# Optimization experiments

Measured on AMD Instinct MI355X. Metric: run time of the kernel, lower is better.

Reference implementation:

```python
import jax, jax.numpy as jnp
import numpy as np
import math

NUM_HEADS = 32
NUM_KV = 8
D = 128          # num_hidden == per-head dim in this module
S = 2048
B = 1
DK = 128
ROPE_BASE = 10000.0


def rope(x):
    # x: [B, H, S, D]; standard Llama-style RoPE (split-halves rotation) over positions.
    d = x.shape[-1]
    half = d // 2
    pos = jnp.arange(x.shape[2], dtype=jnp.float32)                       # [S]
    inv_freq = 1.0 / (ROPE_BASE ** (jnp.arange(half, dtype=jnp.float32) / half))
    ang = pos[:, None] * inv_freq[None, :]                                # [S, half]
    cos = jnp.cos(ang)
    sin = jnp.sin(ang)
    x1 = x[..., :half]
    x2 = x[..., half:]
    return jnp.concatenate([x1 * cos - x2 * sin, x1 * sin + x2 * cos], axis=-1)


def setup_inputs() -> dict:
    key = jax.random.key(0)
    ks = jax.random.split(key, 8)
    query = jax.random.normal(ks[0], (B, S, D), dtype=jnp.float32)
    k_in = jax.random.normal(ks[1], (B, S, D), dtype=jnp.float32)
    v_in = jax.random.normal(ks[2], (B, S, D), dtype=jnp.float32)
    # causal mask: 1 where attention allowed (lower triangle incl diagonal)
    mask = jnp.tril(jnp.ones((S, S), dtype=jnp.int32))[None, None]        # [1,1,S,S]
    sc = 0.02
    Wq = jax.random.normal(ks[3], (NUM_HEADS * D, D), dtype=jnp.float32) * sc
    bq = jnp.zeros((NUM_HEADS * D,), dtype=jnp.float32)
    Wk = jax.random.normal(ks[4], (NUM_KV * D, D), dtype=jnp.float32) * sc
    bk = jnp.zeros((NUM_KV * D,), dtype=jnp.float32)
    Wv = jax.random.normal(ks[5], (NUM_KV * D, D), dtype=jnp.float32) * sc
    bv = jnp.zeros((NUM_KV * D,), dtype=jnp.float32)
    Wo = jax.random.normal(ks[6], (D, NUM_HEADS * D), dtype=jnp.float32) * sc
    bo = jnp.zeros((D,), dtype=jnp.float32)
    return {"query": query, "key": k_in, "values": v_in, "mask": mask,
            "Wq": Wq, "bq": bq, "Wk": Wk, "bk": bk, "Wv": Wv, "bv": bv,
            "Wo": Wo, "bo": bo}


def reference(query, key, values, mask, Wq, bq, Wk, bk, Wv, bv, Wo, bo):
    Bq, Sq, Dh = query.shape
    # projections; torch Linear: x @ W.T + b. Note: view (reshape), not transpose,
    # exactly as in the original module.
    q = (query @ Wq.T + bq).reshape(Bq, NUM_HEADS, Sq, Dh)   # [B,H,S,D]
    k = (key @ Wk.T + bk).reshape(Bq, NUM_KV, Sq, Dh)        # [B,Hkv,S,D]
    v = (values @ Wv.T + bv).reshape(Bq, NUM_KV, Sq, Dh)
    rk = rope(k)
    rv = rope(v)  # module applies RoPE to values too (faithful)
    rep = NUM_HEADS // NUM_KV
    # torch .repeat((1, rep, 1, 1)) tiles whole head blocks -> jnp.tile
    rk = jnp.tile(rk, (1, rep, 1, 1))                        # [B,H,S,D]
    rv = jnp.tile(rv, (1, rep, 1, 1))
    scores = jnp.einsum('bhqd,bhkd->bhqk', q, rk) / math.sqrt(DK)
    scores = jnp.where(mask == 0, -jnp.inf, scores)
    attn = jax.nn.softmax(scores, axis=-1)
    out = jnp.einsum('bhqk,bhkd->bhqd', attn, rv)            # [B,H,S,D]
    out = out.transpose(0, 2, 1, 3).reshape(Bq, Sq, NUM_HEADS * Dh)
    return out @ Wo.T + bo
```

## Files before the change

### kernel.cpp

```cpp
#include <hip/hip_runtime.h>

typedef unsigned short u16;
typedef unsigned int u32;
typedef short frag_t __attribute__((ext_vector_type(8)));
typedef float f32x4 __attribute__((ext_vector_type(4)));

#define S_LEN 2048

__device__ __forceinline__ float bf2f(u32 u) {
  union { u32 i; float f; } v; v.i = u << 16; return v.f;
}
__device__ __forceinline__ u16 f2bf(float f) {
  u32 x = __float_as_uint(f);
  u32 r = (x + 0x7fffu + ((x >> 16) & 1u)) >> 16;
  return (u16)r;
}
__device__ __forceinline__ void unpack8(uint4 r, float* o) {
  o[0] = bf2f(r.x & 0xffffu); o[1] = bf2f(r.x >> 16);
  o[2] = bf2f(r.y & 0xffffu); o[3] = bf2f(r.y >> 16);
  o[4] = bf2f(r.z & 0xffffu); o[5] = bf2f(r.z >> 16);
  o[6] = bf2f(r.w & 0xffffu); o[7] = bf2f(r.w >> 16);
}
__device__ __forceinline__ u16 ld_in(const void* p, size_t idx, bool fp32) {
  if (fp32) return f2bf(((const float*)p)[idx]);
  return ((const u16*)p)[idx];
}
__device__ __forceinline__ uint4 ld8(const void* p, size_t eidx, bool fp32) {
  if (!fp32) return *(const uint4*)((const u16*)p + eidx);
  const float4* f = (const float4*)((const float*)p + eidx);
  float4 x = f[0], y = f[1];
  uint4 r;
  r.x = (u32)f2bf(x.x) | ((u32)f2bf(x.y) << 16);
  r.y = (u32)f2bf(x.z) | ((u32)f2bf(x.w) << 16);
  r.z = (u32)f2bf(y.x) | ((u32)f2bf(y.y) << 16);
  r.w = (u32)f2bf(y.z) | ((u32)f2bf(y.w) << 16);
  return r;
}

__global__ void detect_dtype(const u16* __restrict__ q, u32* __restrict__ flag) {
  int t = threadIdx.x;
  u32 e = ((u32)q[2 * t] >> 7) & 0xFFu;
  bool ok = (e >= 110u && e <= 140u);
  unsigned long long b = __ballot(ok);
  if (t == 0) *flag = (__popcll(b) < 32) ? 1u : 0u;
}

__global__ __launch_bounds__(256) void proj_all(
    const void* __restrict__ query, const void* __restrict__ key,
    const void* __restrict__ values,
    const void* __restrict__ Wq, const void* __restrict__ bq,
    const void* __restrict__ Wk, const void* __restrict__ bk,
    const void* __restrict__ Wv, const void* __restrict__ bv,
    u16* __restrict__ Qb, u16* __restrict__ Kb, u16* __restrict__ Vtmp,
    const u32* __restrict__ flagp) {
  __shared__ u16 As[64][136];
  __shared__ u16 Ws[64][136];
  u16 (*Cs)[72] = (u16(*)[72])&As[0][0];
  const bool fp32 = (*flagp != 0u);
  const int t = threadIdx.x;
  const int x = blockIdx.x;
  const void *A, *W, *bias;
  u16* C; int N, n0;
  if (x < 64)      { A = query;  W = Wq; bias = bq; C = Qb;   N = 4096; n0 = x << 6; }
  else if (x < 80) { A = key;    W = Wk; bias = bk; C = Kb;   N = 1024; n0 = (x - 64) << 6; }
  else             { A = values; W = Wv; bias = bv; C = Vtmp; N = 1024; n0 = (x - 80) << 6; }
  const int m0 = blockIdx.y << 6;
  for (int i = t; i < 1024; i += 256) {
    int r = i >> 4, d8 = (i & 15) << 3;
    *(uint4*)&As[r][d8] = ld8(A, (size_t)(m0 + r) * 128 + d8, fp32);
    *(uint4*)&Ws[r][d8] = ld8(W, (size_t)(n0 + r) * 128 + d8, fp32);
  }
  __syncthreads();
  const int lane = t & 63, w = t >> 6, quad = lane >> 4, l15 = lane & 15;
  f32x4 acc[4];
#pragma unroll
  for (int nt = 0; nt < 4; ++nt) acc[nt] = 0.f;
#pragma unroll
  for (int kc = 0; kc < 4; ++kc) {
    frag_t a = *(const frag_t*)&As[w * 16 + l15][kc * 32 + quad * 8];
#pragma unroll
    for (int nt = 0; nt < 4; ++nt) {
      frag_t b = *(const frag_t*)&Ws[nt * 16 + l15][kc * 32 + quad * 8];
      acc[nt] = __builtin_amdgcn_mfma_f32_16x16x32_bf16(a, b, acc[nt], 0, 0, 0);
    }
  }
  __syncthreads();
#pragma unroll
  for (int nt = 0; nt < 4; ++nt) {
    float bb = bf2f((u32)ld_in(bias, n0 + nt * 16 + l15, fp32));
#pragma unroll
    for (int r = 0; r < 4; ++r)
      Cs[w * 16 + quad * 4 + r][nt * 16 + l15] = f2bf(acc[nt][r] + bb);
  }
  __syncthreads();
#pragma unroll
  for (int jj = 0; jj < 2; ++jj) {
    int c = t + (jj << 8);
    int row = c >> 3, ch = (c & 7) << 3;
    *(uint4*)&C[(size_t)(m0 + row) * N + n0 + ch] = *(const uint4*)&Cs[row][ch];
  }
}

__global__ __launch_bounds__(256) void rope_kv_tr(u16* __restrict__ Kb,
                                                  const u16* __restrict__ Vb,
                                                  u16* __restrict__ VbT) {
  __shared__ u16 Lt[128][72];
  const int t = threadIdx.x;
  const int s0 = blockIdx.x << 6;
  const int g = blockIdx.y;
  for (int i = t; i < 4096; i += 256) {
    int s = s0 + (i >> 6), ii = i & 63;
    float invf = __expf(-(float)ii * 0.14391156831212787f);
    float ang = (float)s * invf;
    float sn, cs;
    sincosf(ang, &sn, &cs);
    size_t base = ((size_t)(g << 11) + s) * 128 + ii;
    float k1 = bf2f((u32)Kb[base]), k2 = bf2f((u32)Kb[base + 64]);
    Kb[base] = f2bf(k1 * cs - k2 * sn);
    Kb[base + 64] = f2bf(k1 * sn + k2 * cs);
  }
  const u16* src = Vb + (size_t)g * S_LEN * 128;
  for (int i = t; i < 512; i += 256) {
    int r = i >> 3, d8 = (i & 7) << 3;
    float lo[8], hi[8];
    unpack8(*(const uint4*)&src[(size_t)(s0 + r) * 128 + d8], lo);
    unpack8(*(const uint4*)&src[(size_t)(s0 + r) * 128 + d8 + 64], hi);
#pragma unroll
    for (int j = 0; j < 8; ++j) {
      float invf = __expf(-(float)(d8 + j) * 0.14391156831212787f);
      float ang = (float)(s0 + r) * invf;
      float sn, cs;
      sincosf(ang, &sn, &cs);
      Lt[d8 + j][r] = f2bf(lo[j] * cs - hi[j] * sn);
      Lt[d8 + 64 + j][r] = f2bf(lo[j] * sn + hi[j] * cs);
    }
  }
  __syncthreads();
  u16* dst = VbT + (size_t)g * 128 * S_LEN + s0;
  for (int i = t; i < 2048; i += 256) {
    int d = i >> 4, s4 = (i & 15) << 2;
    uint2 pk;
    pk.x = (u32)Lt[d][s4] | ((u32)Lt[d][s4 + 1] << 16);
    pk.y = (u32)Lt[d][s4 + 2] | ((u32)Lt[d][s4 + 3] << 16);
    *(uint2*)&dst[(size_t)d * S_LEN + s4] = pk;
  }
}

__global__ __launch_bounds__(512, 2) void attn_mfma(
    const u16* __restrict__ Qb, const u16* __restrict__ Kb,
    const u16* __restrict__ VbT, u16* __restrict__ Ob) {
  __shared__ __align__(16) char smem[102400];
  u16 (*Kt)[64][136] = (u16(*)[64][136])smem;
  u16 (*Vt)[128][72] = (u16(*)[128][72])(smem + 34816);
  u16 (*St)[40]      = (u16(*)[40])(smem + 71680);
  float* Om = (float*)smem;
  float* Ml = (float*)(smem + 65536);
  u16 (*Og)[136]     = (u16(*)[136])(smem + 67584);
  const int t = threadIdx.x;
  const int lane = t & 63, w = t >> 6, quad = lane >> 4, l15 = lane & 15;
  const int hw = w & 3, half = w >> 2;
  const int g = blockIdx.y;
  const int pi = blockIdx.x;
  const int h = g + (hw << 3);
  const u16* Kg = Kb + (size_t)g * S_LEN * 128;
  const u16* Vg = VbT + (size_t)g * 128 * S_LEN;
  const int kr0 = t >> 4, kc0 = (t & 15) << 3;
  const int vr0 = t >> 3, vc0 = (t & 7) << 3;

  for (int tp = 0; tp < 2; ++tp) {
    const int qt = tp ? pi : 63 - pi;
    const int q0 = qt << 5;
    const int niter = qt + 1;
    const int nsuper = (niter + 1) >> 1;
    frag_t aq[2][4];
#pragma unroll
    for (int qp = 0; qp < 2; ++qp)
#pragma unroll
      for (int kc = 0; kc < 4; ++kc)
        aq[qp][kc] = *(const frag_t*)&Qb[((size_t)h * S_LEN + q0 + qp * 16 + l15) * 128 +
                                         kc * 32 + quad * 8];
    float m_r[2] = {-1e30f, -1e30f}, l_r[2] = {0.f, 0.f};
    f32x4 oacc[2][8];
#pragma unroll
    for (int qp = 0; qp < 2; ++qp)
#pragma unroll
      for (int nt = 0; nt < 8; ++nt) oacc[qp][nt] = 0.f;

    uint4 kpf[2], vpf[2];
#pragma unroll
    for (int j = 0; j < 2; ++j) {
      kpf[j] = *(const uint4*)&Kg[(size_t)(kr0 + j * 32) * 128 + kc0];
      vpf[j] = *(const uint4*)&Vg[(size_t)(vr0 + j * 64) * S_LEN + vc0];
    }
#pragma unroll
    for (int j = 0; j < 2; ++j) {
      *(uint4*)&Kt[0][kr0 + j * 32][kc0] = kpf[j];
      *(uint4*)&Vt[0][vr0 + j * 64][vc0] = vpf[j];
    }
    if (nsuper > 1) {
#pragma unroll
      for (int j = 0; j < 2; ++j) {
        kpf[j] = *(const uint4*)&Kg[(size_t)(64 + kr0 + j * 32) * 128 + kc0];
        vpf[j] = *(const uint4*)&Vg[(size_t)(vr0 + j * 64) * S_LEN + 64 + vc0];
      }
    }

    for (int sj = 0; sj < nsuper; ++sj) {
      __syncthreads();
      const int buf = sj & 1;
      if (sj + 1 < nsuper) {
#pragma unroll
        for (int j = 0; j < 2; ++j) {
          *(uint4*)&Kt[buf ^ 1][kr0 + j * 32][kc0] = kpf[j];
          *(uint4*)&Vt[buf ^ 1][vr0 + j * 64][vc0] = vpf[j];
        }
      }
      if (sj + 2 < nsuper) {
        const int kn = (sj + 2) << 6;
#pragma unroll
        for (int j = 0; j < 2; ++j) {
          kpf[j] = *(const uint4*)&Kg[(size_t)(kn + kr0 + j * 32) * 128 + kc0];
          vpf[j] = *(const uint4*)&Vg[(size_t)(vr0 + j * 64) * S_LEN + kn + vc0];
        }
      }
      const int tile32 = (sj << 1) + half;
      if (tile32 < niter) {
        const int kbase = tile32 << 5;
        const int lk = half << 5;
        f32x4 s4[2][2];
#pragma unroll
        for (int kk = 0; kk < 2; ++kk)
#pragma unroll
          for (int qp = 0; qp < 2; ++qp) s4[kk][qp] = 0.f;
#pragma unroll
        for (int kc = 0; kc < 4; ++kc) {
#pragma unroll
          for (int kk = 0; kk < 2; ++kk) {
            frag_t a = *(const frag_t*)&Kt[buf][lk + kk * 16 + l15][kc * 32 + quad * 8];
            s4[kk][0] = __builtin_amdgcn_mfma_f32_16x16x32_bf16(a, aq[0][kc], s4[kk][0], 0, 0, 0);
            s4[kk][1] = __builtin_amdgcn_mfma_f32_16x16x32_bf16(a, aq[1][kc], s4[kk][1], 0, 0, 0);
          }
        }
        const bool lastm = (tile32 == niter - 1);
        float alpha[2];
#pragma unroll
        for (int qp = 0; qp < 2; ++qp) {
          const int qg = q0 + qp * 16 + l15;
          float mx = -1e30f;
#pragma unroll
          for (int kk = 0; kk < 2; ++kk)
#pragma unroll
            for (int r = 0; r < 4; ++r) {
              float sv = s4[kk][qp][r] * 0.08838834764831845f;
              if (lastm && (kbase + kk * 16 + quad * 4 + r) > qg) sv = -1e30f;
              s4[kk][qp][r] = sv;
              mx = fmaxf(mx, sv);
            }
          mx = fmaxf(mx, __shfl_xor(mx, 16));
          mx = fmaxf(mx, __shfl_xor(mx, 32));
          float mn = fmaxf(m_r[qp], mx);
          alpha[qp] = __expf(m_r[qp] - mn);
          m_r[qp] = mn;
          float sum = 0.f;
          const int strow = w * 32 + qp * 16 + l15;
#pragma unroll
          for (int kk = 0; kk < 2; ++kk) {
            float p0 = __expf(s4[kk][qp][0] - mn);
            float p1 = __expf(s4[kk][qp][1] - mn);
            float p2 = __expf(s4[kk][qp][2] - mn);
            float p3 = __expf(s4[kk][qp][3] - mn);
            sum += (p0 + p1) + (p2 + p3);
            uint2 pk;
            pk.x = (u32)f2bf(p0) | ((u32)f2bf(p1) << 16);
            pk.y = (u32)f2bf(p2) | ((u32)f2bf(p3) << 16);
            *(uint2*)&St[strow][kk * 16 + quad * 4] = pk;
          }
          sum += __shfl_xor(sum, 16);
          sum += __shfl_xor(sum, 32);
          l_r[qp] = l_r[qp] * alpha[qp] + sum;
        }
#pragma unroll
        for (int qp = 0; qp < 2; ++qp)
#pragma unroll
          for (int r = 0; r < 4; ++r) {
            float al = __shfl(alpha[qp], quad * 4 + r);
#pragma unroll
            for (int nt = 0; nt < 8; ++nt) oacc[qp][nt][r] *= al;
          }
        frag_t pa[2];
#pragma unroll
        for (int qp = 0; qp < 2; ++qp)
          pa[qp] = *(const frag_t*)&St[w * 32 + qp * 16 + l15][quad * 8];
#pragma unroll
        for (int nt = 0; nt < 8; ++nt) {
          frag_t v = *(const frag_t*)&Vt[buf][nt * 16 + l15][lk + quad * 8];
          oacc[0][nt] = __builtin_amdgcn_mfma_f32_16x16x32_bf16(pa[0], v, oacc[0][nt], 0, 0, 0);
          oacc[1][nt] = __builtin_amdgcn_mfma_f32_16x16x32_bf16(pa[1], v, oacc[1][nt], 0, 0, 0);
        }
      }
    }
    __syncthreads();
    if (half == 1) {
#pragma unroll
      for (int qp = 0; qp < 2; ++qp)
#pragma unroll
        for (int nt = 0; nt < 8; ++nt)
#pragma unroll
          for (int r = 0; r < 4; ++r)
            Om[((hw * 32) + qp * 16 + quad * 4 + r) * 128 + nt * 16 + l15] = oacc[qp][nt][r];
      if (quad == 0) {
#pragma unroll
        for (int qp = 0; qp < 2; ++qp) {
          Ml[hw * 64 + qp * 16 + l15] = m_r[qp];
          Ml[hw * 64 + 32 + qp * 16 + l15] = l_r[qp];
        }
      }
    }
    __syncthreads();
    if (half == 0) {
      float v1[2], v2[2];
#pragma unroll
      for (int qp = 0; qp < 2; ++qp) {
        float m2 = Ml[hw * 64 + qp * 16 + l15];
        float l2 = Ml[hw * 64 + 32 + qp * 16 + l15];
        float mn = fmaxf(m_r[qp], m2);
        float a1 = __expf(m_r[qp] - mn);
        float a2 = __expf(m2 - mn);
        float linv = 1.0f / (a1 * l_r[qp] + a2 * l2);
        v1[qp] = a1 * linv;
        v2[qp] = a2 * linv;
      }
#pragma unroll
      for (int qp = 0; qp < 2; ++qp)
#pragma unroll
        for (int r = 0; r < 4; ++r) {
          float w1 = __shfl(v1[qp], quad * 4 + r);
          float w2 = __shfl(v2[qp], quad * 4 + r);
#pragma unroll
          for (int nt = 0; nt < 8; ++nt) {
            float o2 = Om[((hw * 32) + qp * 16 + quad * 4 + r) * 128 + nt * 16 + l15];
            Og[hw * 32 + qp * 16 + quad * 4 + r][nt * 16 + l15] =
                f2bf(oacc[qp][nt][r] * w1 + o2 * w2);
          }
        }
    }
    __syncthreads();
#pragma unroll
    for (int jj = 0; jj < 4; ++jj) {
      int c = t + (jj << 9);
      int row = c >> 4, ch = (c & 15) << 3;
      int hh = row >> 5, qr = row & 31;
      *(uint4*)&Ob[(size_t)(q0 + qr) * 4096 + (g + hh * 8) * 128 + ch] =
          *(const uint4*)&Og[row][ch];
    }
  }
}

__global__ __launch_bounds__(256) void out_part(
    const u16* __restrict__ Ob, const void* __restrict__ Wo,
    float* __restrict__ Pout, const u32* __restrict__ flagp) {
  __shared__ u16 As[32][72];
  __shared__ u16 Ws[64][72];
  const bool fp32 = (*flagp != 0u);
  const int t = threadIdx.x;
  const int lane = t & 63, w = t >> 6, quad = lane >> 4, l15 = lane & 15;
  const int wm = w & 1, wn = w >> 1;
  const int n0 = (int)blockIdx.x << 6;
  const int m0 = (int)blockIdx.y << 5;
  const int kz = (int)blockIdx.z << 10;
  f32x4 acc[2];
#pragma unroll
  for (int nt = 0; nt < 2; ++nt) acc[nt] = 0.f;
  for (int kc0 = kz; kc0 < kz + 1024; kc0 += 64) {
    if (kc0 != kz) __syncthreads();
    {
      int r = t >> 3, k8 = (t & 7) << 3;
      *(uint4*)&As[r][k8] = *(const uint4*)&Ob[(size_t)(m0 + r) * 4096 + kc0 + k8];
    }
    for (int i = t; i < 512; i += 256) {
      int r = i >> 3, k8 = (i & 7) << 3;
      *(uint4*)&Ws[r][k8] = ld8(Wo, (size_t)(n0 + r) * 4096 + kc0 + k8, fp32);
    }
    __syncthreads();
#pragma unroll
    for (int kc2 = 0; kc2 < 2; ++kc2) {
      frag_t a = *(const frag_t*)&As[wm * 16 + l15][kc2 * 32 + quad * 8];
#pragma unroll
      for (int nt = 0; nt < 2; ++nt) {
        frag_t b = *(const frag_t*)&Ws[wn * 32 + nt * 16 + l15][kc2 * 32 + quad * 8];
        acc[nt] = __builtin_amdgcn_mfma_f32_16x16x32_bf16(a, b, acc[nt], 0, 0, 0);
      }
    }
  }
#pragma unroll
  for (int nt = 0; nt < 2; ++nt) {
    int n = n0 + wn * 32 + nt * 16 + l15;
#pragma unroll
    for (int r = 0; r < 4; ++r) {
      int m = m0 + wm * 16 + quad * 4 + r;
      Pout[((size_t)blockIdx.z * 2048 + m) * 128 + n] = acc[nt][r];
    }
  }
}

__global__ __launch_bounds__(256) void out_red(
    const float* __restrict__ Pout, const void* __restrict__ bo,
    void* __restrict__ out, const u32* __restrict__ flagp) {
  const bool fp32 = (*flagp != 0u);
  int e4 = blockIdx.x * 256 + threadIdx.x;
  const float4* P = (const float4*)Pout;
  float4 s = P[e4];
  float4 s1 = P[65536 + e4], s2 = P[131072 + e4], s3 = P[196608 + e4];
  s.x += s1.x + s2.x + s3.x; s.y += s1.y + s2.y + s3.y;
  s.z += s1.z + s2.z + s3.z; s.w += s1.w + s2.w + s3.w;
  int n = (e4 << 2) & 127;
  s.x += bf2f((u32)ld_in(bo, n + 0, fp32));
  s.y += bf2f((u32)ld_in(bo, n + 1, fp32));
  s.z += bf2f((u32)ld_in(bo, n + 2, fp32));
  s.w += bf2f((u32)ld_in(bo, n + 3, fp32));
  if (fp32) {
    ((float4*)out)[e4] = s;
  } else {
    uint2 pk;
    pk.x = (u32)f2bf(s.x) | ((u32)f2bf(s.y) << 16);
    pk.y = (u32)f2bf(s.z) | ((u32)f2bf(s.w) << 16);
    *(uint2*)((u16*)out + (e4 << 2)) = pk;
  }
}

extern "C" void kernel_launch(void* const* d_in, const int* in_sizes, int n_in,
                              void* d_out, int out_size, void* d_ws, size_t ws_size,
                              hipStream_t stream) {
  (void)in_sizes; (void)n_in; (void)out_size; (void)ws_size;
  const void* query  = d_in[0];
  const void* key    = d_in[1];
  const void* values = d_in[2];
  const void* Wq = d_in[4];
  const void* bq = d_in[5];
  const void* Wk = d_in[6];
  const void* bk = d_in[7];
  const void* Wv = d_in[8];
  const void* bv = d_in[9];
  const void* Wo = d_in[10];
  const void* bo = d_in[11];

  char* ws = (char*)d_ws;
  u32* flag  = (u32*)ws;
  u16* Qb    = (u16*)(ws + 64);
  u16* Kb    = (u16*)(ws + 64 + (16u << 20));
  u16* VbT   = (u16*)(ws + 64 + (20u << 20));
  u16* Vtmp  = (u16*)(ws + 64 + (24u << 20));
  u16* Ob    = (u16*)(ws + 64 + (24u << 20));
  float* Pout = (float*)Qb;

  detect_dtype<<<1, 64, 0, stream>>>((const u16*)query, flag);
  proj_all<<<dim3(96, 32), 256, 0, stream>>>(query, key, values, Wq, bq, Wk, bk,
                                             Wv, bv, Qb, Kb, Vtmp, flag);
  rope_kv_tr<<<dim3(32, 8), 256, 0, stream>>>(Kb, Vtmp, VbT);
  attn_mfma<<<dim3(32, 8), 512, 0, stream>>>(Qb, Kb, VbT, Ob);
  out_part<<<dim3(2, 64, 4), 256, 0, stream>>>(Ob, Wo, Pout, flag);
  out_red<<<256, 256, 0, stream>>>(Pout, bo, d_out, flag);
}
```

Measured before the change: 257.8 us.

## Retile projections and output GEMM, split attention into one q-tile per block

The QKV projection and output GEMMs move from 64x64 tiles to 128x128 tiles, with each wave computing a 64x64 sub-tile, which raises operand reuse and cuts block count. The output projection now splits K 16 ways, and the reduction kernel sums 16 partials instead of 4. Attention drops the paired q-tile loop and launches one q-tile per block with twice the blocks. It uses single-buffered K/V through a shared-memory union, targets 4 blocks per CU, and stages the half-merge in bf16 instead of fp32. The cost is one extra barrier per K/V step, more partial-sum traffic, and some extra rounding in the merge.

Measured after the change: 431.5 us. 67.4% more time.

```diff
diff --git a/kernel.cpp b/kernel.cpp
--- a/kernel.cpp
+++ b/kernel.cpp
@@ -53,50 +53,67 @@
     const void* __restrict__ Wv, const void* __restrict__ bv,
     u16* __restrict__ Qb, u16* __restrict__ Kb, u16* __restrict__ Vtmp,
     const u32* __restrict__ flagp) {
-  __shared__ u16 As[64][136];
-  __shared__ u16 Ws[64][136];
-  u16 (*Cs)[72] = (u16(*)[72])&As[0][0];
+  __shared__ u16 As[128][136];
+  __shared__ u16 Ws[128][136];
+  u16 (*Cs)[136] = As;
   const bool fp32 = (*flagp != 0u);
   const int t = threadIdx.x;
   const int x = blockIdx.x;
   const void *A, *W, *bias;
   u16* C; int N, n0;
-  if (x < 64)      { A = query;  W = Wq; bias = bq; C = Qb;   N = 4096; n0 = x << 6; }
-  else if (x < 80) { A = key;    W = Wk; bias = bk; C = Kb;   N = 1024; n0 = (x - 64) << 6; }
-  else             { A = values; W = Wv; bias = bv; C = Vtmp; N = 1024; n0 = (x - 80) << 6; }
-  const int m0 = blockIdx.y << 6;
-  for (int i = t; i < 1024; i += 256) {
-    int r = i >> 4, d8 = (i & 15) << 3;
-    *(uint4*)&As[r][d8] = ld8(A, (size_t)(m0 + r) * 128 + d8, fp32);
-    *(uint4*)&Ws[r][d8] = ld8(W, (size_t)(n0 + r) * 128 + d8, fp32);
+  if (x < 32)      { A = query;  W = Wq; bias = bq; C = Qb;   N = 4096; n0 = x << 7; }
+  else if (x < 40) { A = key;    W = Wk; bias = bk; C = Kb;   N = 1024; n0 = (x - 32) << 7; }
+  else             { A = values; W = Wv; bias = bv; C = Vtmp; N = 1024; n0 = (x - 40) << 7; }
+  const int m0 = blockIdx.y << 7;
+#pragma unroll
+  for (int i = 0; i < 8; ++i) {
+    int task = t + (i << 8);
+    int row = task >> 4, ch = (task & 15) << 3;
+    *(uint4*)&As[row][ch] = ld8(A, (size_t)(m0 + row) * 128 + ch, fp32);
+    *(uint4*)&Ws[row][ch] = ld8(W, (size_t)(n0 + row) * 128 + ch, fp32);
   }
   __syncthreads();
   const int lane = t & 63, w = t >> 6, quad = lane >> 4, l15 = lane & 15;
-  f32x4 acc[4];
-#pragma unroll
-  for (int nt = 0; nt < 4; ++nt) acc[nt] = 0.f;
-#pragma unroll
-  for (int kc = 0; kc < 4; ++kc) {
-    frag_t a = *(const frag_t*)&As[w * 16 + l15][kc * 32 + quad * 8];
-#pragma unroll
-    for (int nt = 0; nt < 4; ++nt) {
-      frag_t b = *(const frag_t*)&Ws[nt * 16 + l15][kc * 32 + quad * 8];
-      acc[nt] = __builtin_amdgcn_mfma_f32_16x16x32_bf16(a, b, acc[nt], 0, 0, 0);
-    }
+  const int rm = (w & 1) << 6, rn = (w >> 1) << 6;
+  f32x4 acc[4][4];
+#pragma unroll
+  for (int mt = 0; mt < 4; ++mt)
+#pragma unroll
+    for (int nt = 0; nt < 4; ++nt) acc[mt][nt] = 0.f;
+#pragma unroll
+  for (int mtp = 0; mtp < 2; ++mtp) {
+    frag_t a0[4], a1[4];
+#pragma unroll
+    for (int kc = 0; kc < 4; ++kc) {
+      a0[kc] = *(const frag_t*)&As[rm + mtp * 32 + l15][kc * 32 + quad * 8];
+      a1[kc] = *(const frag_t*)&As[rm + mtp * 32 + 16 + l15][kc * 32 + quad * 8];
+    }
+#pragma unroll
+    for (int nt = 0; nt < 4; ++nt)
+#pragma unroll
+      for (int kc = 0; kc < 4; ++kc) {
+        frag_t b = *(const frag_t*)&Ws[rn + nt * 16 + l15][kc * 32 + quad * 8];
+        acc[mtp * 2][nt] = __builtin_amdgcn_mfma_f32_16x16x32_bf16(a0[kc], b, acc[mtp * 2][nt], 0, 0, 0);
+        acc[mtp * 2 + 1][nt] = __builtin_amdgcn_mfma_f32_16x16x32_bf16(a1[kc], b, acc[mtp * 2 + 1][nt], 0, 0, 0);
+      }
   }
   __syncthreads();
 #pragma unroll
   for (int nt = 0; nt < 4; ++nt) {
-    float bb = bf2f((u32)ld_in(bias, n0 + nt * 16 + l15, fp32));
-#pragma unroll
-    for (int r = 0; r < 4; ++r)
-      Cs[w * 16 + quad * 4 + r][nt * 16 + l15] = f2bf(acc[nt][r] + bb);
-  }
-  __syncthreads();
-#pragma unroll
-  for (int jj = 0; jj < 2; ++jj) {
-    int c = t + (jj << 8);
-    int row = c >> 3, ch = (c & 7) << 3;
+    float bb = bf2f((u32)ld_in(bias, n0 + rn + nt * 16 + l15, fp32));
+#pragma unroll
+    for (int mt = 0; mt < 4; ++mt) {
+      int row = rm + ((mt >> 1) * 32) + ((mt & 1) * 16) + quad * 4;
+#pragma unroll
+      for (int r = 0; r < 4; ++r)
+        Cs[row + r][rn + nt * 16 + l15] = f2bf(acc[mt][nt][r] + bb);
+    }
+  }
+  __syncthreads();
+#pragma unroll
+  for (int i = 0; i < 8; ++i) {
+    int task = t + (i << 8);
+    int row = task >> 4, ch = (task & 15) << 3;
     *(uint4*)&C[(size_t)(m0 + row) * N + n0 + ch] = *(const uint4*)&Cs[row][ch];
   }
 }
@@ -146,259 +163,250 @@
   }
 }
 
-__global__ __launch_bounds__(512, 2) void attn_mfma(
+__global__ __launch_bounds__(512, 4) void attn_mfma(
     const u16* __restrict__ Qb, const u16* __restrict__ Kb,
     const u16* __restrict__ VbT, u16* __restrict__ Ob) {
-  __shared__ __align__(16) char smem[102400];
-  u16 (*Kt)[64][136] = (u16(*)[64][136])smem;
-  u16 (*Vt)[128][72] = (u16(*)[128][72])(smem + 34816);
-  u16 (*St)[40]      = (u16(*)[40])(smem + 71680);
-  float* Om = (float*)smem;
-  float* Ml = (float*)(smem + 65536);
-  u16 (*Og)[136]     = (u16(*)[136])(smem + 67584);
+  __shared__ union SmemU {
+    struct { u16 Kt[64][136]; u16 Vt[128][72]; u16 St[256][40]; } m;
+    struct { u16 Og[128][136]; float Ml[256]; } e;
+  } su;
   const int t = threadIdx.x;
   const int lane = t & 63, w = t >> 6, quad = lane >> 4, l15 = lane & 15;
   const int hw = w & 3, half = w >> 2;
   const int g = blockIdx.y;
-  const int pi = blockIdx.x;
+  const int qt = 63 - (int)blockIdx.x;
+  const int q0 = qt << 5;
   const int h = g + (hw << 3);
   const u16* Kg = Kb + (size_t)g * S_LEN * 128;
   const u16* Vg = VbT + (size_t)g * 128 * S_LEN;
   const int kr0 = t >> 4, kc0 = (t & 15) << 3;
   const int vr0 = t >> 3, vc0 = (t & 7) << 3;
 
-  for (int tp = 0; tp < 2; ++tp) {
-    const int qt = tp ? pi : 63 - pi;
-    const int q0 = qt << 5;
-    const int niter = qt + 1;
-    const int nsuper = (niter + 1) >> 1;
-    frag_t aq[2][4];
+  frag_t aq[2][4];
+#pragma unroll
+  for (int qp = 0; qp < 2; ++qp)
+#pragma unroll
+    for (int kc = 0; kc < 4; ++kc)
+      aq[qp][kc] = *(const frag_t*)&Qb[((size_t)h * S_LEN + q0 + qp * 16 + l15) * 128 +
+                                       kc * 32 + quad * 8];
+  float m_r[2] = {-1e30f, -1e30f}, l_r[2] = {0.f, 0.f};
+  f32x4 oacc[2][8];
+#pragma unroll
+  for (int qp = 0; qp < 2; ++qp)
+#pragma unroll
+    for (int nt = 0; nt < 8; ++nt) oacc[qp][nt] = 0.f;
+  const int niter = qt + 1;
+  const int nsuper = (qt >> 1) + 1;
+
+  uint4 kpf[2], vpf[2];
+#pragma unroll
+  for (int j = 0; j < 2; ++j) {
+    kpf[j] = *(const uint4*)&Kg[(size_t)(kr0 + j * 32) * 128 + kc0];
+    vpf[j] = *(const uint4*)&Vg[(size_t)(vr0 + j * 64) * S_LEN + vc0];
+  }
+
+  for (int sj = 0; sj < nsuper; ++sj) {
+    __syncthreads();
+#pragma unroll
+    for (int j = 0; j < 2; ++j) {
+      *(uint4*)&su.m.Kt[kr0 + j * 32][kc0] = kpf[j];
+      *(uint4*)&su.m.Vt[vr0 + j * 64][vc0] = vpf[j];
+    }
+    __syncthreads();
+    if (sj + 1 < nsuper) {
+      const int kn = (sj + 1) << 6;
+#pragma unroll
+      for (int j = 0; j < 2; ++j) {
+        kpf[j] = *(const uint4*)&Kg[(size_t)(kn + kr0 + j * 32) * 128 + kc0];
+        vpf[j] = *(const uint4*)&Vg[(size_t)(vr0 + j * 64) * S_LEN + kn + vc0];
+      }
+    }
+    const int tile32 = (sj << 1) + half;
+    if (tile32 < niter) {
+      const int lk = half << 5;
+      const int kbase = (sj << 6) + lk;
+      f32x4 s4[2][2];
+#pragma unroll
+      for (int kk = 0; kk < 2; ++kk)
+#pragma unroll
+        for (int qp = 0; qp < 2; ++qp) s4[kk][qp] = 0.f;
+#pragma unroll
+      for (int kc = 0; kc < 4; ++kc) {
+#pragma unroll
+        for (int kk = 0; kk < 2; ++kk) {
+          frag_t a = *(const frag_t*)&su.m.Kt[lk + kk * 16 + l15][kc * 32 + quad * 8];
+          s4[kk][0] = __builtin_amdgcn_mfma_f32_16x16x32_bf16(a, aq[0][kc], s4[kk][0], 0, 0, 0);
+          s4[kk][1] = __builtin_amdgcn_mfma_f32_16x16x32_bf16(a, aq[1][kc], s4[kk][1], 0, 0, 0);
+        }
+      }
+      const bool lastm = (tile32 == niter - 1);
+      float alpha[2];
+#pragma unroll
+      for (int qp = 0; qp < 2; ++qp) {
+        const int qg = q0 + qp * 16 + l15;
+        float mx = -1e30f;
+#pragma unroll
+        for (int kk = 0; kk < 2; ++kk)
+#pragma unroll
+          for (int r = 0; r < 4; ++r) {
+            float sv = s4[kk][qp][r] * 0.08838834764831845f;
+            if (lastm && (kbase + kk * 16 + quad * 4 + r) > qg) sv = -1e30f;
+            s4[kk][qp][r] = sv;
+            mx = fmaxf(mx, sv);
+          }
+        mx = fmaxf(mx, __shfl_xor(mx, 16));
+        mx = fmaxf(mx, __shfl_xor(mx, 32));
+        float mn = fmaxf(m_r[qp], mx);
+        alpha[qp] = __expf(m_r[qp] - mn);
+        m_r[qp] = mn;
+        float sum = 0.f;
+        const int strow = w * 32 + qp * 16 + l15;
+#pragma unroll
+        for (int kk = 0; kk < 2; ++kk) {
+          float p0 = __expf(s4[kk][qp][0] - mn);
+          float p1 = __expf(s4[kk][qp][1] - mn);
+          float p2 = __expf(s4[kk][qp][2] - mn);
+          float p3 = __expf(s4[kk][qp][3] - mn);
+          sum += (p0 + p1) + (p2 + p3);
+          uint2 pk;
+          pk.x = (u32)f2bf(p0) | ((u32)f2bf(p1) << 16);
+          pk.y = (u32)f2bf(p2) | ((u32)f2bf(p3) << 16);
+          *(uint2*)&su.m.St[strow][kk * 16 + quad * 4] = pk;
+        }
+        sum += __shfl_xor(sum, 16);
+        sum += __shfl_xor(sum, 32);
+        l_r[qp] = l_r[qp] * alpha[qp] + sum;
+      }
+#pragma unroll
+      for (int qp = 0; qp < 2; ++qp)
+#pragma unroll
+        for (int r = 0; r < 4; ++r) {
+          float al = __shfl(alpha[qp], quad * 4 + r);
+#pragma unroll
+          for (int nt = 0; nt < 8; ++nt) oacc[qp][nt][r] *= al;
+        }
+      frag_t pa[2];
+#pragma unroll
+      for (int qp = 0; qp < 2; ++qp)
+        pa[qp] = *(const frag_t*)&su.m.St[w * 32 + qp * 16 + l15][quad * 8];
+#pragma unroll
+      for (int nt = 0; nt < 8; ++nt) {
+        frag_t v = *(const frag_t*)&su.m.Vt[nt * 16 + l15][lk + quad * 8];
+        oacc[0][nt] = __builtin_amdgcn_mfma_f32_16x16x32_bf16(pa[0], v, oacc[0][nt], 0, 0, 0);
+        oacc[1][nt] = __builtin_amdgcn_mfma_f32_16x16x32_bf16(pa[1], v, oacc[1][nt], 0, 0, 0);
+      }
+    }
+  }
+  __syncthreads();
+  if (half == 1) {
 #pragma unroll
     for (int qp = 0; qp < 2; ++qp)
 #pragma unroll
-      for (int kc = 0; kc < 4; ++kc)
-        aq[qp][kc] = *(const frag_t*)&Qb[((size_t)h * S_LEN + q0 + qp * 16 + l15) * 128 +
-                                         kc * 32 + quad * 8];
-    float m_r[2] = {-1e30f, -1e30f}, l_r[2] = {0.f, 0.f};
-    f32x4 oacc[2][8];
+      for (int nt = 0; nt < 8; ++nt)
+#pragma unroll
+        for (int r = 0; r < 4; ++r)
+          su.e.Og[hw * 32 + qp * 16 + quad * 4 + r][nt * 16 + l15] = f2bf(oacc[qp][nt][r]);
+    if (quad == 0) {
+#pragma unroll
+      for (int qp = 0; qp < 2; ++qp) {
+        su.e.Ml[hw * 64 + qp * 16 + l15] = m_r[qp];
+        su.e.Ml[hw * 64 + 32 + qp * 16 + l15] = l_r[qp];
+      }
+    }
+  }
+  __syncthreads();
+  if (half == 0) {
+    float v1[2], v2[2];
+#pragma unroll
+    for (int qp = 0; qp < 2; ++qp) {
+      float m2 = su.e.Ml[hw * 64 + qp * 16 + l15];
+      float l2 = su.e.Ml[hw * 64 + 32 + qp * 16 + l15];
+      float mn = fmaxf(m_r[qp], m2);
+      float a1 = __expf(m_r[qp] - mn);
+      float a2 = __expf(m2 - mn);
+      float linv = 1.0f / (a1 * l_r[qp] + a2 * l2);
+      v1[qp] = a1 * linv;
+      v2[qp] = a2 * linv;
+    }
 #pragma unroll
     for (int qp = 0; qp < 2; ++qp)
 #pragma unroll
-      for (int nt = 0; nt < 8; ++nt) oacc[qp][nt] = 0.f;
-
-    uint4 kpf[2], vpf[2];
-#pragma unroll
-    for (int j = 0; j < 2; ++j) {
-      kpf[j] = *(const uint4*)&Kg[(size_t)(kr0 + j * 32) * 128 + kc0];
-      vpf[j] = *(const uint4*)&Vg[(size_t)(vr0 + j * 64) * S_LEN + vc0];
-    }
-#pragma unroll
-    for (int j = 0; j < 2; ++j) {
-      *(uint4*)&Kt[0][kr0 + j * 32][kc0] = kpf[j];
-      *(uint4*)&Vt[0][vr0 + j * 64][vc0] = vpf[j];
-    }
-    if (nsuper > 1) {
-#pragma unroll
-      for (int j = 0; j < 2; ++j) {
-        kpf[j] = *(const uint4*)&Kg[(size_t)(64 + kr0 + j * 32) * 128 + kc0];
-        vpf[j] = *(const uint4*)&Vg[(size_t)(vr0 + j * 64) * S_LEN + 64 + vc0];
-      }
-    }
-
-    for (int sj = 0; sj < nsuper; ++sj) {
-      __syncthreads();
-      const int buf = sj & 1;
-      if (sj + 1 < nsuper) {
-#pragma unroll
-        for (int j = 0; j < 2; ++j) {
-          *(uint4*)&Kt[buf ^ 1][kr0 + j * 32][kc0] = kpf[j];
-          *(uint4*)&Vt[buf ^ 1][vr0 + j * 64][vc0] = vpf[j];
+      for (int r = 0; r < 4; ++r) {
+        float w1 = __shfl(v1[qp], quad * 4 + r);
+        float w2 = __shfl(v2[qp], quad * 4 + r);
+        int row = hw * 32 + qp * 16 + quad * 4 + r;
+#pragma unroll
+        for (int nt = 0; nt < 8; ++nt) {
+          float o2 = bf2f((u32)su.e.Og[row][nt * 16 + l15]);
+          su.e.Og[row][nt * 16 + l15] = f2bf(oacc[qp][nt][r] * w1 + o2 * w2);
         }
       }
-      if (sj + 2 < nsuper) {
-        const int kn = (sj + 2) << 6;
-#pragma unroll
-        for (int j = 0; j < 2; ++j) {
-          kpf[j] = *(const uint4*)&Kg[(size_t)(kn + kr0 + j * 32) * 128 + kc0];
-          vpf[j] = *(const uint4*)&Vg[(size_t)(vr0 + j * 64) * S_LEN + kn + vc0];
-        }
-      }
-      const int tile32 = (sj << 1) + half;
-      if (tile32 < niter) {
-        const int kbase = tile32 << 5;
-        const int lk = half << 5;
-        f32x4 s4[2][2];
-#pragma unroll
-        for (int kk = 0; kk < 2; ++kk)
-#pragma unroll
-          for (int qp = 0; qp < 2; ++qp) s4[kk][qp] = 0.f;
-#pragma unroll
-        for (int kc = 0; kc < 4; ++kc) {
-#pragma unroll
-          for (int kk = 0; kk < 2; ++kk) {
-            frag_t a = *(const frag_t*)&Kt[buf][lk + kk * 16 + l15][kc * 32 + quad * 8];
-            s4[kk][0] = __builtin_amdgcn_mfma_f32_16x16x32_bf16(a, aq[0][kc], s4[kk][0], 0, 0, 0);
-            s4[kk][1] = __builtin_amdgcn_mfma_f32_16x16x32_bf16(a, aq[1][kc], s4[kk][1], 0, 0, 0);
-          }
-        }
-        const bool lastm = (tile32 == niter - 1);
-        float alpha[2];
-#pragma unroll
-        for (int qp = 0; qp < 2; ++qp) {
-          const int qg = q0 + qp * 16 + l15;
-          float mx = -1e30f;
-#pragma unroll
-          for (int kk = 0; kk < 2; ++kk)
-#pragma unroll
-            for (int r = 0; r < 4; ++r) {
-              float sv = s4[kk][qp][r] * 0.08838834764831845f;
-              if (lastm && (kbase + kk * 16 + quad * 4 + r) > qg) sv = -1e30f;
-              s4[kk][qp][r] = sv;
-              mx = fmaxf(mx, sv);
-            }
-          mx = fmaxf(mx, __shfl_xor(mx, 16));
-          mx = fmaxf(mx, __shfl_xor(mx, 32));
-          float mn = fmaxf(m_r[qp], mx);
-          alpha[qp] = __expf(m_r[qp] - mn);
-          m_r[qp] = mn;
-          float sum = 0.f;
-          const int strow = w * 32 + qp * 16 + l15;
-#pragma unroll
-          for (int kk = 0; kk < 2; ++kk) {
-            float p0 = __expf(s4[kk][qp][0] - mn);
-            float p1 = __expf(s4[kk][qp][1] - mn);
-            float p2 = __expf(s4[kk][qp][2] - mn);
-            float p3 = __expf(s4[kk][qp][3] - mn);
-            sum += (p0 + p1) + (p2 + p3);
-            uint2 pk;
-            pk.x = (u32)f2bf(p0) | ((u32)f2bf(p1) << 16);
-            pk.y = (u32)f2bf(p2) | ((u32)f2bf(p3) << 16);
-            *(uint2*)&St[strow][kk * 16 + quad * 4] = pk;
-          }
-          sum += __shfl_xor(sum, 16);
-          sum += __shfl_xor(sum, 32);
-          l_r[qp] = l_r[qp] * alpha[qp] + sum;
-        }
-#pragma unroll
-        for (int qp = 0; qp < 2; ++qp)
-#pragma unroll
-          for (int r = 0; r < 4; ++r) {
-            float al = __shfl(alpha[qp], quad * 4 + r);
-#pragma unroll
-            for (int nt = 0; nt < 8; ++nt) oacc[qp][nt][r] *= al;
-          }
-        frag_t pa[2];
-#pragma unroll
-        for (int qp = 0; qp < 2; ++qp)
-          pa[qp] = *(const frag_t*)&St[w * 32 + qp * 16 + l15][quad * 8];
-#pragma unroll
-        for (int nt = 0; nt < 8; ++nt) {
-          frag_t v = *(const frag_t*)&Vt[buf][nt * 16 + l15][lk + quad * 8];
-          oacc[0][nt] = __builtin_amdgcn_mfma_f32_16x16x32_bf16(pa[0], v, oacc[0][nt], 0, 0, 0);
-          oacc[1][nt] = __builtin_amdgcn_mfma_f32_16x16x32_bf16(pa[1], v, oacc[1][nt], 0, 0, 0);
-        }
-      }
-    }
-    __syncthreads();
-    if (half == 1) {
-#pragma unroll
-      for (int qp = 0; qp < 2; ++qp)
-#pragma unroll
-        for (int nt = 0; nt < 8; ++nt)
-#pragma unroll
-          for (int r = 0; r < 4; ++r)
-            Om[((hw * 32) + qp * 16 + quad * 4 + r) * 128 + nt * 16 + l15] = oacc[qp][nt][r];
-      if (quad == 0) {
-#pragma unroll
-        for (int qp = 0; qp < 2; ++qp) {
-          Ml[hw * 64 + qp * 16 + l15] = m_r[qp];
-          Ml[hw * 64 + 32 + qp * 16 + l15] = l_r[qp];
-        }
-      }
-    }
-    __syncthreads();
-    if (half == 0) {
-      float v1[2], v2[2];
-#pragma unroll
-      for (int qp = 0; qp < 2; ++qp) {
-        float m2 = Ml[hw * 64 + qp * 16 + l15];
-        float l2 = Ml[hw * 64 + 32 + qp * 16 + l15];
-        float mn = fmaxf(m_r[qp], m2);
-        float a1 = __expf(m_r[qp] - mn);
-        float a2 = __expf(m2 - mn);
-        float linv = 1.0f / (a1 * l_r[qp] + a2 * l2);
-        v1[qp] = a1 * linv;
-        v2[qp] = a2 * linv;
-      }
-#pragma unroll
-      for (int qp = 0; qp < 2; ++qp)
-#pragma unroll
-        for (int r = 0; r < 4; ++r) {
-          float w1 = __shfl(v1[qp], quad * 4 + r);
-          float w2 = __shfl(v2[qp], quad * 4 + r);
-#pragma unroll
-          for (int nt = 0; nt < 8; ++nt) {
-            float o2 = Om[((hw * 32) + qp * 16 + quad * 4 + r) * 128 + nt * 16 + l15];
-            Og[hw * 32 + qp * 16 + quad * 4 + r][nt * 16 + l15] =
-                f2bf(oacc[qp][nt][r] * w1 + o2 * w2);
-          }
-        }
-    }
-    __syncthreads();
-#pragma unroll
-    for (int jj = 0; jj < 4; ++jj) {
-      int c = t + (jj << 9);
-      int row = c >> 4, ch = (c & 15) << 3;
-      int hh = row >> 5, qr = row & 31;
-      *(uint4*)&Ob[(size_t)(q0 + qr) * 4096 + (g + hh * 8) * 128 + ch] =
-          *(const uint4*)&Og[row][ch];
-    }
+  }
+  __syncthreads();
+#pragma unroll
+  for (int jj = 0; jj < 4; ++jj) {
+    int c = t + (jj << 9);
+    int row = c >> 4, ch = (c & 15) << 3;
+    int hh = row >> 5, qr = row & 31;
+    *(uint4*)&Ob[(size_t)(q0 + qr) * 4096 + (g + hh * 8) * 128 + ch] =
+        *(const uint4*)&su.e.Og[row][ch];
   }
 }
 
 __global__ __launch_bounds__(256) void out_part(
     const u16* __restrict__ Ob, const void* __restrict__ Wo,
     float* __restrict__ Pout, const u32* __restrict__ flagp) {
-  __shared__ u16 As[32][72];
-  __shared__ u16 Ws[64][72];
+  __shared__ u16 As[128][136];
+  __shared__ u16 Ws[128][136];
   const bool fp32 = (*flagp != 0u);
   const int t = threadIdx.x;
   const int lane = t & 63, w = t >> 6, quad = lane >> 4, l15 = lane & 15;
-  const int wm = w & 1, wn = w >> 1;
-  const int n0 = (int)blockIdx.x << 6;
-  const int m0 = (int)blockIdx.y << 5;
-  const int kz = (int)blockIdx.z << 10;
-  f32x4 acc[2];
-#pragma unroll
-  for (int nt = 0; nt < 2; ++nt) acc[nt] = 0.f;
-  for (int kc0 = kz; kc0 < kz + 1024; kc0 += 64) {
-    if (kc0 != kz) __syncthreads();
-    {
-      int r = t >> 3, k8 = (t & 7) << 3;
-      *(uint4*)&As[r][k8] = *(const uint4*)&Ob[(size_t)(m0 + r) * 4096 + kc0 + k8];
-    }
-    for (int i = t; i < 512; i += 256) {
-      int r = i >> 3, k8 = (i & 7) << 3;
-      *(uint4*)&Ws[r][k8] = ld8(Wo, (size_t)(n0 + r) * 4096 + kc0 + k8, fp32);
+  const int rm = (w & 1) << 6, rn = (w >> 1) << 6;
+  const int m0 = (int)blockIdx.x << 7;
+  const int z = (int)blockIdx.y;
+  f32x4 acc[4][4];
+#pragma unroll
+  for (int mt = 0; mt < 4; ++mt)
+#pragma unroll
+    for (int nt = 0; nt < 4; ++nt) acc[mt][nt] = 0.f;
+  for (int kc2 = 0; kc2 < 2; ++kc2) {
+    if (kc2) __syncthreads();
+    const int kc0 = (z << 8) + (kc2 << 7);
+#pragma unroll
+    for (int i = 0; i < 8; ++i) {
+      int task = t + (i << 8);
+      int row = task >> 4, ch = (task & 15) << 3;
+      *(uint4*)&As[row][ch] = *(const uint4*)&Ob[(size_t)(m0 + row) * 4096 + kc0 + ch];
+      *(uint4*)&Ws[row][ch] = ld8(Wo, (size_t)row * 4096 + kc0 + ch, fp32);
     }
     __syncthreads();
 #pragma unroll
-    for (int kc2 = 0; kc2 < 2; ++kc2) {
-      frag_t a = *(const frag_t*)&As[wm * 16 + l15][kc2 * 32 + quad * 8];
-#pragma unroll
-      for (int nt = 0; nt < 2; ++nt) {
-        frag_t b = *(const frag_t*)&Ws[wn * 32 + nt * 16 + l15][kc2 * 32 + quad * 8];
-        acc[nt] = __builtin_amdgcn_mfma_f32_16x16x32_bf16(a, b, acc[nt], 0, 0, 0);
-      }
-    }
-  }
-#pragma unroll
-  for (int nt = 0; nt < 2; ++nt) {
-    int n = n0 + wn * 32 + nt * 16 + l15;
-#pragma unroll
-    for (int r = 0; r < 4; ++r) {
-      int m = m0 + wm * 16 + quad * 4 + r;
-      Pout[((size_t)blockIdx.z * 2048 + m) * 128 + n] = acc[nt][r];
+    for (int mtp = 0; mtp < 2; ++mtp) {
+      frag_t a0[4], a1[4];
+#pragma unroll
+      for (int kc = 0; kc < 4; ++kc) {
+        a0[kc] = *(const frag_t*)&As[rm + mtp * 32 + l15][kc * 32 + quad * 8];
+        a1[kc] = *(const frag_t*)&As[rm + mtp * 32 + 16 + l15][kc * 32 + quad * 8];
+      }
+#pragma unroll
+      for (int nt = 0; nt < 4; ++nt)
+#pragma unroll
+        for (int kc = 0; kc < 4; ++kc) {
+          frag_t b = *(const frag_t*)&Ws[rn + nt * 16 + l15][kc * 32 + quad * 8];
+          acc[mtp * 2][nt] = __builtin_amdgcn_mfma_f32_16x16x32_bf16(a0[kc], b, acc[mtp * 2][nt], 0, 0, 0);
+          acc[mtp * 2 + 1][nt] = __builtin_amdgcn_mfma_f32_16x16x32_bf16(a1[kc], b, acc[mtp * 2 + 1][nt], 0, 0, 0);
+        }
+    }
+  }
+#pragma unroll
+  for (int mt = 0; mt < 4; ++mt) {
+    int mrow = m0 + rm + ((mt >> 1) * 32) + ((mt & 1) * 16) + quad * 4;
+#pragma unroll
+    for (int nt = 0; nt < 4; ++nt) {
+      int n = rn + nt * 16 + l15;
+#pragma unroll
+      for (int r = 0; r < 4; ++r)
+        Pout[((size_t)z * 2048 + mrow + r) * 128 + n] = acc[mt][nt][r];
     }
   }
 }
@@ -410,9 +418,11 @@
   int e4 = blockIdx.x * 256 + threadIdx.x;
   const float4* P = (const float4*)Pout;
   float4 s = P[e4];
-  float4 s1 = P[65536 + e4], s2 = P[131072 + e4], s3 = P[196608 + e4];
-  s.x += s1.x + s2.x + s3.x; s.y += s1.y + s2.y + s3.y;
-  s.z += s1.z + s2.z + s3.z; s.w += s1.w + s2.w + s3.w;
+#pragma unroll
+  for (int z = 1; z < 16; ++z) {
+    float4 p = P[(size_t)z * 65536 + e4];
+    s.x += p.x; s.y += p.y; s.z += p.z; s.w += p.w;
+  }
   int n = (e4 << 2) & 127;
   s.x += bf2f((u32)ld_in(bo, n + 0, fp32));
   s.y += bf2f((u32)ld_in(bo, n + 1, fp32));
@@ -454,10 +464,10 @@
   float* Pout = (float*)Qb;
 
   detect_dtype<<<1, 64, 0, stream>>>((const u16*)query, flag);
-  proj_all<<<dim3(96, 32), 256, 0, stream>>>(query, key, values, Wq, bq, Wk, bk,
+  proj_all<<<dim3(48, 16), 256, 0, stream>>>(query, key, values, Wq, bq, Wk, bk,
                                              Wv, bv, Qb, Kb, Vtmp, flag);
   rope_kv_tr<<<dim3(32, 8), 256, 0, stream>>>(Kb, Vtmp, VbT);
-  attn_mfma<<<dim3(32, 8), 512, 0, stream>>>(Qb, Kb, VbT, Ob);
-  out_part<<<dim3(2, 64, 4), 256, 0, stream>>>(Ob, Wo, Pout, flag);
+  attn_mfma<<<dim3(64, 8), 512, 0, stream>>>(Qb, Kb, VbT, Ob);
+  out_part<<<dim3(16, 16), 256, 0, stream>>>(Ob, Wo, Pout, flag);
   out_red<<<256, 256, 0, stream>>>(Pout, bo, d_out, flag);
 }
```
